# Optimization experiments

Hardware: AMD Instinct MI355X
Metric: run time of the kernel (lower is better)

The kernel has to match this reference:

```python
import jax, jax.numpy as jnp
import numpy as np

N = 750_000      # total nodes (10,000 graphs x 75 superpixels)
E = 6_000_000    # directed edges (avg degree 8)
G = 10_000       # number of graphs
NINP, H, HFC, NCLS = 2, 64, 32, 10
BN_EPS = 1e-5


def setup_inputs() -> dict:
    key = jax.random.key(0)
    ks = jax.random.split(key, 12)
    x = jax.random.normal(ks[0], (N, NINP), dtype=jnp.float32)
    edge_index = jax.random.randint(ks[1], (2, E), 0, N, dtype=jnp.int32)
    batch = jnp.sort(jax.random.randint(ks[2], (N,), 0, G, dtype=jnp.int32))
    def glorot(k, shape):
        fan_in, fan_out = shape
        s = jnp.sqrt(6.0 / (fan_in + fan_out)).astype(jnp.float32)
        return jax.random.uniform(k, shape, jnp.float32, -s, s)
    return {
        "x": x, "edge_index": edge_index, "batch": batch,
        "W1": glorot(ks[3], (NINP, H)), "b1": jnp.zeros((H,), jnp.float32),
        "W2": glorot(ks[4], (H, H)),    "b2": jnp.zeros((H,), jnp.float32),
        "W3": glorot(ks[5], (H, H)),    "b3": jnp.zeros((H,), jnp.float32),
        "gamma": jnp.ones((H,), jnp.float32), "beta": jnp.zeros((H,), jnp.float32),
        "fcW1": glorot(ks[6], (H, HFC)),  "fcb1": jnp.zeros((HFC,), jnp.float32),
        "fcW2": glorot(ks[7], (HFC, NCLS)), "fcb2": jnp.zeros((NCLS,), jnp.float32),
    }


def reference(x, edge_index, batch, W1, b1, W2, b2, W3, b3,
              gamma, beta, fcW1, fcb1, fcW2, fcb2):
    n = x.shape[0]
    loop = jnp.arange(n, dtype=edge_index.dtype)
    src = jnp.concatenate([edge_index[0], loop])   # [E+N] self-loops added
    dst = jnp.concatenate([edge_index[1], loop])
    # symmetric GCN normalization: deg from destination with unit edge weights
    deg = jax.ops.segment_sum(jnp.ones_like(dst, jnp.float32), dst, num_segments=n)
    dinv = jnp.where(deg > 0, jax.lax.rsqrt(deg), 0.0)
    norm = (dinv[src] * dinv[dst])[:, None]        # [E+N, 1]

    def gcn_conv(h, W, b):
        h = h @ W                                   # linear transform first (small K)
        msg = h[src] * norm                         # gather + normalize
        return jax.ops.segment_sum(msg, dst, num_segments=n) + b  # scatter-add

    h = jax.nn.relu(gcn_conv(x, W1, b1))
    h = jax.nn.relu(gcn_conv(h, W2, b2))
    h = jax.nn.relu(gcn_conv(h, W3, b3))

    # global mean pool over graphs
    sums = jax.ops.segment_sum(h, batch, num_segments=G)
    cnts = jax.ops.segment_sum(jnp.ones((n, 1), jnp.float32), batch, num_segments=G)
    pooled = sums / jnp.maximum(cnts, 1.0)          # [G, H]

    # BatchNorm1d (training mode: batch statistics, biased variance)
    mean = pooled.mean(axis=0)
    var = pooled.var(axis=0)
    hbn = (pooled - mean) * jax.lax.rsqrt(var + BN_EPS) * gamma + beta

    h = jax.nn.relu(hbn @ fcW1 + fcb1)
    logits = h @ fcW2 + fcb2
    return jax.nn.log_softmax(logits, axis=1)
```

## Files before the change

kernel.cpp:

```cpp
#include <hip/hip_runtime.h>
#include <hip/hip_fp16.h>

#define HDIM 64
#define HFC 32
#define NCLS 10
#define DT32 32
#define DT64 64

#define NBUCK 256
#define BSH   12
#define BUCKN 4096
#define EPT   16
#define CHUNK 4096
#define CAPSH 16
#define CAP   (1 << CAPSH)

__device__ inline __half2 u2h2(unsigned int u) {
    __half2 r;
    *reinterpret_cast<unsigned int*>(&r) = u;
    return r;
}
__device__ inline unsigned int h22u(__half2 h) {
    return *reinterpret_cast<unsigned int*>(&h);
}

__device__ inline __half2 h2relu(__half2 a) {
    unsigned int ua = h22u(a), uz = 0u, r;
    asm("v_pk_max_f16 %0, %1, %2" : "=v"(r) : "v"(ua), "v"(uz));
    return u2h2(r);
}

__device__ inline float fdot2u(unsigned int a, unsigned int b, float c) {
#if __has_builtin(__builtin_amdgcn_fdot2)
    typedef _Float16 f16x2 __attribute__((ext_vector_type(2)));
    union U { unsigned int u; f16x2 h; };
    U ua, ub; ua.u = a; ub.u = b;
    return __builtin_amdgcn_fdot2(ua.h, ub.h, c, false);
#else
    float2 fa = __half22float2(u2h2(a));
    float2 fb = __half22float2(u2h2(b));
    return fmaf(fa.x, fb.x, fmaf(fa.y, fb.y, c));
#endif
}


__global__ void k_initcur(int* __restrict__ gcur) {
    gcur[threadIdx.x] = threadIdx.x << CAPSH;
}

__global__ __launch_bounds__(256) void k_split(const int* __restrict__ src,
                                               const int* __restrict__ dst,
                                               int* __restrict__ gcur,
                                               unsigned int* __restrict__ part, int E) {
    __shared__ int cnt[NBUCK];
    __shared__ int off[NBUCK];
    cnt[threadIdx.x] = 0;
    __syncthreads();
    int base = blockIdx.x * CHUNK + threadIdx.x;
    int s16[EPT], d16[EPT], b16[EPT];
    #pragma unroll
    for (int i = 0; i < EPT; ++i) {
        int e = base + i * 256;
        bool ok = e < E;
        s16[i] = ok ? src[e] : 0;
        d16[i] = ok ? dst[e] : 0;
        b16[i] = ok ? (d16[i] >> BSH) : -1;
        if (ok) atomicAdd(&cnt[b16[i]], 1);
    }
    __syncthreads();
    {
        int c = cnt[threadIdx.x];
        off[threadIdx.x] = c ? atomicAdd(&gcur[threadIdx.x], c) : 0;
    }
    __syncthreads();
    #pragma unroll
    for (int i = 0; i < EPT; ++i) {
        if (b16[i] >= 0) {
            int slot = atomicAdd(&off[b16[i]], 1);
            part[slot] = ((unsigned)(d16[i] & (BUCKN - 1)) << 20) | (unsigned)s16[i];
        }
    }
}

__global__ __launch_bounds__(256) void k_build(const unsigned int* __restrict__ part,
                                               const int* __restrict__ gcur,
                                               unsigned int* __restrict__ begdeg,
                                               int* __restrict__ col, int n) {
    __shared__ int cnt[BUCKN];
    __shared__ int tmp[256];
    const int b = blockIdx.x;
    const int s = b << CAPSH, t = gcur[b];
    const int nodeBase = b << BSH;
    for (int i = threadIdx.x; i < BUCKN; i += 256) cnt[i] = 0;
    __syncthreads();
    for (int e = s + threadIdx.x; e < t; e += 256) {
        int local = (int)(part[e] >> 20);
        atomicAdd(&cnt[local], 1);
    }
    __syncthreads();
    int my[16]; int sum = 0;
    #pragma unroll
    for (int i = 0; i < 16; ++i) { my[i] = cnt[threadIdx.x * 16 + i]; sum += my[i]; }
    tmp[threadIdx.x] = sum; __syncthreads();
    for (int o = 1; o < 256; o <<= 1) {
        int v = ((int)threadIdx.x >= o) ? tmp[threadIdx.x - o] : 0;
        __syncthreads();
        tmp[threadIdx.x] += v;
        __syncthreads();
    }
    int run = tmp[threadIdx.x] - sum + s;
    __syncthreads();
    #pragma unroll
    for (int i = 0; i < 16; ++i) {
        int local = threadIdx.x * 16 + i;
        int node = nodeBase + local;
        int c = my[i];
        cnt[local] = run;
        if (node < n) begdeg[node] = ((unsigned)c << 24) | (unsigned)run;
        run += c;
    }
    __syncthreads();
    for (int e = s + threadIdx.x; e < t; e += 256) {
        unsigned int pe = part[e];
        int local = (int)(pe >> 20);
        int p = atomicAdd(&cnt[local], 1);
        col[p] = (int)(pe & 0xFFFFFu);
    }
}


__global__ void k_xs(const float* __restrict__ x, const unsigned int* __restrict__ begdeg,
                     unsigned int* __restrict__ xsh, int n) {
    int i = blockIdx.x * blockDim.x + threadIdx.x;
    if (i >= n) return;
    unsigned int bd = begdeg[i];
    float dv = rsqrtf((float)(bd >> 24) + 1.0f);
    float2 v = reinterpret_cast<const float2*>(x)[i];
    xsh[i] = h22u(__floats2half2_rn(v.x * dv, v.y * dv));
}

__global__ void k_gather1(const unsigned int* __restrict__ begdeg, const int* __restrict__ col,
                          const unsigned int* __restrict__ xsh,
                          uint2* __restrict__ aggd, int n) {
    int d = blockIdx.x * blockDim.x + threadIdx.x;
    if (d >= n) return;
    unsigned int bd = begdeg[d];
    int e0 = (int)(bd & 0xFFFFFFu);
    int deg = (int)(bd >> 24);
    int e1 = e0 + deg;
    float dv = rsqrtf((float)deg + 1.0f);
    float2 v = __half22float2(u2h2(xsh[d]));
    float a0 = v.x, a1 = v.y;
    int e = e0;
    for (; e + 4 <= e1; e += 4) {
        int c0 = col[e], c1 = col[e + 1], c2 = col[e + 2], c3 = col[e + 3];
        float2 w0 = __half22float2(u2h2(xsh[c0]));
        float2 w1 = __half22float2(u2h2(xsh[c1]));
        float2 w2 = __half22float2(u2h2(xsh[c2]));
        float2 w3 = __half22float2(u2h2(xsh[c3]));
        a0 += w0.x + w1.x + w2.x + w3.x;
        a1 += w0.y + w1.y + w2.y + w3.y;
    }
    for (; e < e1; ++e) {
        float2 w = __half22float2(u2h2(xsh[col[e]]));
        a0 += w.x; a1 += w.y;
    }
    uint2 o;
    o.x = h22u(__floats2half2_rn(a0 * dv, a1 * dv));
    o.y = h22u(__floats2half2_rn(dv, 0.0f));
    aggd[d] = o;
}

__global__ __launch_bounds__(256) void k_layer12(
        const unsigned int* __restrict__ begdeg, const int* __restrict__ col,
        const uint2* __restrict__ aggd,
        const float* __restrict__ W1, const float* __restrict__ b1,
        const float* __restrict__ W2, const float* __restrict__ b2,
        __half* __restrict__ out, int n) {
    __shared__ unsigned int sWp[HDIM / 2][HDIM];
    __shared__ float sB2[HDIM];
    __shared__ float sW1a[HDIM], sW1b[HDIM], sB1[HDIM];
    __shared__ unsigned int sAgg[DT64][HDIM / 2];
    __shared__ __half sOut[DT64][HDIM];

    for (int i = threadIdx.x; i < (HDIM / 2) * HDIM; i += 256) {
        int k2 = i >> 6, f = i & 63;
        sWp[k2][f] = h22u(__floats2half2_rn(W2[(2 * k2) * HDIM + f], W2[(2 * k2 + 1) * HDIM + f]));
    }
    if (threadIdx.x < HDIM) {
        sW1a[threadIdx.x] = W1[threadIdx.x];
        sW1b[threadIdx.x] = W1[HDIM + threadIdx.x];
        sB1[threadIdx.x] = b1[threadIdx.x];
        sB2[threadIdx.x] = b2[threadIdx.x];
    }
    __syncthreads();

    const int base = blockIdx.x * DT64;
    const int nValid = min(DT64, n - base);
    const int nd = threadIdx.x >> 2;
    const int q  = threadIdx.x & 3;
    const int node = base + nd;

    __half2 w1a2[8], w1b2[8], bb2[8];
    #pragma unroll
    for (int j = 0; j < 8; ++j) {
        int f = q * 16 + 2 * j;
        w1a2[j] = __floats2half2_rn(sW1a[f], sW1a[f + 1]);
        w1b2[j] = __floats2half2_rn(sW1b[f], sW1b[f + 1]);
        bb2[j]  = __floats2half2_rn(sB1[f], sB1[f + 1]);
    }

    if (nd < nValid) {
        __half2 acc[8];
        uint2 sv = aggd[node];
        __half2 zz = u2h2(sv.x);
        __half2 zx2 = __low2half2(zz), zy2 = __high2half2(zz);
        __half2 sd2 = __low2half2(u2h2(sv.y));
        #pragma unroll
        for (int j = 0; j < 8; ++j) {
            __half2 t = __hfma2(zx2, w1a2[j], __hfma2(zy2, w1b2[j], bb2[j]));
            acc[j] = __hmul2(h2relu(t), sd2);
        }
        unsigned int bd = begdeg[node];
        int e0 = (int)(bd & 0xFFFFFFu);
        int e1 = e0 + (int)(bd >> 24);
        int e = e0;
        for (; e + 4 <= e1; e += 4) {
            int c0 = col[e], c1 = col[e + 1], c2 = col[e + 2], c3 = col[e + 3];
            uint2 v0 = aggd[c0];
            uint2 v1 = aggd[c1];
            uint2 v2 = aggd[c2];
            uint2 v3 = aggd[c3];
            __half2 z0 = u2h2(v0.x), z1 = u2h2(v1.x), z2 = u2h2(v2.x), z3 = u2h2(v3.x);
            __half2 x0 = __low2half2(z0), y0 = __high2half2(z0), d0 = __low2half2(u2h2(v0.y));
            __half2 x1 = __low2half2(z1), y1 = __high2half2(z1), d1 = __low2half2(u2h2(v1.y));
            __half2 x2 = __low2half2(z2), y2 = __high2half2(z2), d2 = __low2half2(u2h2(v2.y));
            __half2 x3 = __low2half2(z3), y3 = __high2half2(z3), d3 = __low2half2(u2h2(v3.y));
            #pragma unroll
            for (int j = 0; j < 8; ++j) {
                __half2 t0 = __hfma2(x0, w1a2[j], __hfma2(y0, w1b2[j], bb2[j]));
                acc[j] = __hfma2(h2relu(t0), d0, acc[j]);
                __half2 t1 = __hfma2(x1, w1a2[j], __hfma2(y1, w1b2[j], bb2[j]));
                acc[j] = __hfma2(h2relu(t1), d1, acc[j]);
                __half2 t2 = __hfma2(x2, w1a2[j], __hfma2(y2, w1b2[j], bb2[j]));
                acc[j] = __hfma2(h2relu(t2), d2, acc[j]);
                __half2 t3 = __hfma2(x3, w1a2[j], __hfma2(y3, w1b2[j], bb2[j]));
                acc[j] = __hfma2(h2relu(t3), d3, acc[j]);
            }
        }
        for (; e < e1; ++e) {
            uint2 v0 = aggd[col[e]];
            __half2 z0 = u2h2(v0.x);
            __half2 x0 = __low2half2(z0), y0 = __high2half2(z0), d0 = __low2half2(u2h2(v0.y));
            #pragma unroll
            for (int j = 0; j < 8; ++j) {
                __half2 t0 = __hfma2(x0, w1a2[j], __hfma2(y0, w1b2[j], bb2[j]));
                acc[j] = __hfma2(h2relu(t0), d0, acc[j]);
            }
        }
        #pragma unroll
        for (int j = 0; j < 8; ++j) acc[j] = __hmul2(acc[j], sd2);
        uint4 o0, o1;
        o0.x = h22u(acc[0]); o0.y = h22u(acc[1]); o0.z = h22u(acc[2]); o0.w = h22u(acc[3]);
        o1.x = h22u(acc[4]); o1.y = h22u(acc[5]); o1.z = h22u(acc[6]); o1.w = h22u(acc[7]);
        uint4* sa = reinterpret_cast<uint4*>(&sAgg[nd][q * 8]);
        sa[0] = o0; sa[1] = o1;
    }
    __syncthreads();

    {
        const int f  = threadIdx.x & 63;
        const int ng = threadIdx.x >> 6;
        for (int ii = ng; ii < DT64; ii += 4) {
            int onode = base + ii;
            if (onode >= n) break;
            float acc = sB2[f];
            #pragma unroll
            for (int k2 = 0; k2 < HDIM / 2; ++k2)
                acc = fdot2u(sAgg[ii][k2], sWp[k2][f], acc);
            unsigned int bd = begdeg[onode];
            float sc = rsqrtf((float)(bd >> 24) + 1.0f);
            sOut[ii][f] = __float2half(fmaxf(acc, 0.0f) * sc);
        }
    }
    __syncthreads();

    if (nd < nValid) {
        const uint4* so = reinterpret_cast<const uint4*>(&sOut[nd][q * 16]);
        uint4* go = reinterpret_cast<uint4*>(out + (long long)node * HDIM + q * 16);
        go[0] = so[0];
        go[1] = so[1];
    }
}

__global__ __launch_bounds__(256) void k_layer64(
        const unsigned int* __restrict__ begdeg, const int* __restrict__ col,
        const __half* __restrict__ hs,
        const float* __restrict__ W, const float* __restrict__ b,
        const int* __restrict__ batchArr,
        float* __restrict__ pooled, int n) {
    __shared__ unsigned int sWp[HDIM / 2][HDIM];
    __shared__ float sB[HDIM];
    __shared__ unsigned int sAgg[DT32][HDIM / 2];
    __shared__ __half sOut[DT32][HDIM];
    __shared__ int sGid[DT32];

    for (int i = threadIdx.x; i < (HDIM / 2) * HDIM; i += 256) {
        int k2 = i >> 6, f = i & 63;
        sWp[k2][f] = h22u(__floats2half2_rn(W[(2 * k2) * HDIM + f], W[(2 * k2 + 1) * HDIM + f]));
    }
    if (threadIdx.x < HDIM) sB[threadIdx.x] = b[threadIdx.x];

    const int base = blockIdx.x * DT32;
    const int nValid = min(DT32, n - base);
    const int nd = threadIdx.x >> 3;
    const int q  = threadIdx.x & 7;
    const int node = base + nd;

    if (threadIdx.x < DT32)
        sGid[threadIdx.x] = (threadIdx.x < nValid) ? batchArr[base + threadIdx.x] : -1;

    if (nd < nValid) {
        const uint4* rows = reinterpret_cast<const uint4*>(hs);
        uint4 v = rows[(long long)node * 8 + q];
        __half2 a0 = u2h2(v.x), a1 = u2h2(v.y), a2 = u2h2(v.z), a3 = u2h2(v.w);
        __half2 b0 = u2h2(0u), b1 = u2h2(0u), b2 = u2h2(0u), b3 = u2h2(0u);
        unsigned int bd = begdeg[node];
        int e0 = (int)(bd & 0xFFFFFFu);
        int deg = (int)(bd >> 24);
        int e1 = e0 + deg;
        int e = e0;
        for (; e + 8 <= e1; e += 8) {
            int c0 = col[e], c1 = col[e + 1], c2 = col[e + 2], c3 = col[e + 3];
            int c4 = col[e + 4], c5 = col[e + 5], c6 = col[e + 6], c7 = col[e + 7];
            uint4 w0 = rows[(long long)c0 * 8 + q];
            uint4 w1 = rows[(long long)c1 * 8 + q];
            uint4 w2 = rows[(long long)c2 * 8 + q];
            uint4 w3 = rows[(long long)c3 * 8 + q];
            uint4 w4 = rows[(long long)c4 * 8 + q];
            uint4 w5 = rows[(long long)c5 * 8 + q];
            uint4 w6 = rows[(long long)c6 * 8 + q];
            uint4 w7 = rows[(long long)c7 * 8 + q];
            a0 = __hadd2(a0, u2h2(w0.x)); a1 = __hadd2(a1, u2h2(w0.y));
            a2 = __hadd2(a2, u2h2(w0.z)); a3 = __hadd2(a3, u2h2(w0.w));
            b0 = __hadd2(b0, u2h2(w1.x)); b1 = __hadd2(b1, u2h2(w1.y));
            b2 = __hadd2(b2, u2h2(w1.z)); b3 = __hadd2(b3, u2h2(w1.w));
            a0 = __hadd2(a0, u2h2(w2.x)); a1 = __hadd2(a1, u2h2(w2.y));
            a2 = __hadd2(a2, u2h2(w2.z)); a3 = __hadd2(a3, u2h2(w2.w));
            b0 = __hadd2(b0, u2h2(w3.x)); b1 = __hadd2(b1, u2h2(w3.y));
            b2 = __hadd2(b2, u2h2(w3.z)); b3 = __hadd2(b3, u2h2(w3.w));
            a0 = __hadd2(a0, u2h2(w4.x)); a1 = __hadd2(a1, u2h2(w4.y));
            a2 = __hadd2(a2, u2h2(w4.z)); a3 = __hadd2(a3, u2h2(w4.w));
            b0 = __hadd2(b0, u2h2(w5.x)); b1 = __hadd2(b1, u2h2(w5.y));
            b2 = __hadd2(b2, u2h2(w5.z)); b3 = __hadd2(b3, u2h2(w5.w));
            a0 = __hadd2(a0, u2h2(w6.x)); a1 = __hadd2(a1, u2h2(w6.y));
            a2 = __hadd2(a2, u2h2(w6.z)); a3 = __hadd2(a3, u2h2(w6.w));
            b0 = __hadd2(b0, u2h2(w7.x)); b1 = __hadd2(b1, u2h2(w7.y));
            b2 = __hadd2(b2, u2h2(w7.z)); b3 = __hadd2(b3, u2h2(w7.w));
        }
        for (; e + 4 <= e1; e += 4) {
            int c0 = col[e], c1 = col[e + 1], c2 = col[e + 2], c3 = col[e + 3];
            uint4 w0 = rows[(long long)c0 * 8 + q];
            uint4 w1 = rows[(long long)c1 * 8 + q];
            uint4 w2 = rows[(long long)c2 * 8 + q];
            uint4 w3 = rows[(long long)c3 * 8 + q];
            a0 = __hadd2(a0, u2h2(w0.x)); a1 = __hadd2(a1, u2h2(w0.y));
            a2 = __hadd2(a2, u2h2(w0.z)); a3 = __hadd2(a3, u2h2(w0.w));
            b0 = __hadd2(b0, u2h2(w1.x)); b1 = __hadd2(b1, u2h2(w1.y));
            b2 = __hadd2(b2, u2h2(w1.z)); b3 = __hadd2(b3, u2h2(w1.w));
            a0 = __hadd2(a0, u2h2(w2.x)); a1 = __hadd2(a1, u2h2(w2.y));
            a2 = __hadd2(a2, u2h2(w2.z)); a3 = __hadd2(a3, u2h2(w2.w));
            b0 = __hadd2(b0, u2h2(w3.x)); b1 = __hadd2(b1, u2h2(w3.y));
            b2 = __hadd2(b2, u2h2(w3.z)); b3 = __hadd2(b3, u2h2(w3.w));
        }
        for (; e < e1; ++e) {
            uint4 w = rows[(long long)col[e] * 8 + q];
            a0 = __hadd2(a0, u2h2(w.x)); a1 = __hadd2(a1, u2h2(w.y));
            a2 = __hadd2(a2, u2h2(w.z)); a3 = __hadd2(a3, u2h2(w.w));
        }
        a0 = __hadd2(a0, b0); a1 = __hadd2(a1, b1);
        a2 = __hadd2(a2, b2); a3 = __hadd2(a3, b3);
        float dv = rsqrtf((float)deg + 1.0f);
        float2 f0 = __half22float2(a0), f1 = __half22float2(a1);
        float2 f2 = __half22float2(a2), f3 = __half22float2(a3);
        uint4 o;
        o.x = h22u(__floats2half2_rn(f0.x * dv, f0.y * dv));
        o.y = h22u(__floats2half2_rn(f1.x * dv, f1.y * dv));
        o.z = h22u(__floats2half2_rn(f2.x * dv, f2.y * dv));
        o.w = h22u(__floats2half2_rn(f3.x * dv, f3.y * dv));
        *reinterpret_cast<uint4*>(&sAgg[nd][q * 4]) = o;
    }
    __syncthreads();

    {
        const int f  = threadIdx.x & 63;
        const int ng = threadIdx.x >> 6;
        for (int ii = ng; ii < DT32; ii += 4) {
            int onode = base + ii;
            if (onode >= n) break;
            float acc = sB[f];
            #pragma unroll
            for (int k2 = 0; k2 < HDIM / 2; ++k2)
                acc = fdot2u(sAgg[ii][k2], sWp[k2][f], acc);
            sOut[ii][f] = __float2half(fmaxf(acc, 0.0f));
        }
    }
    __syncthreads();

    if (threadIdx.x < HDIM) {
        int f = threadIdx.x;
        float acc = 0.0f;
        int prev = sGid[0];
        for (int ii = 0; ii < nValid; ++ii) {
            int g = sGid[ii];
            if (g != prev) {
                if (prev >= 0) atomicAdd(&pooled[(long long)prev * HDIM + f], acc);
                acc = 0.0f; prev = g;
            }
            acc += __half2float(sOut[ii][f]);
        }
        if (prev >= 0) atomicAdd(&pooled[(long long)prev * HDIM + f], acc);
    }
}


__global__ void k_start(const int* __restrict__ batch, int* __restrict__ startArr,
                        int n, int G) {
    int g = blockIdx.x * blockDim.x + threadIdx.x;
    if (g > G) return;
    int lo = 0, hi = n;
    while (lo < hi) {
        int mid = (lo + hi) >> 1;
        if (batch[mid] < g) lo = mid + 1; else hi = mid;
    }
    startArr[g] = lo;
}

__global__ void k_bnstats(const float* __restrict__ pooled, const int* __restrict__ startArr,
                          const float* __restrict__ gamma, const float* __restrict__ beta,
                          float* __restrict__ scale, float* __restrict__ shift, int G) {
    int f = blockIdx.x;
    __shared__ float ss[256], ss2[256];
    float s = 0.0f, s2 = 0.0f;
    for (int g = threadIdx.x; g < G; g += blockDim.x) {
        float c = (float)(startArr[g + 1] - startArr[g]);
        float v = pooled[(long long)g * HDIM + f] / fmaxf(c, 1.0f);
        s += v; s2 += v * v;
    }
    ss[threadIdx.x] = s; ss2[threadIdx.x] = s2;
    __syncthreads();
    for (int off = 128; off > 0; off >>= 1) {
        if (threadIdx.x < off) {
            ss[threadIdx.x]  += ss[threadIdx.x + off];
            ss2[threadIdx.x] += ss2[threadIdx.x + off];
        }
        __syncthreads();
    }
    if (threadIdx.x == 0) {
        float mean = ss[0] / (float)G;
        float var  = ss2[0] / (float)G - mean * mean;
        float rstd = rsqrtf(var + 1e-5f);
        float sc = gamma[f] * rstd;
        scale[f] = sc;
        shift[f] = beta[f] - mean * sc;
    }
}

__global__ void k_head(const float* __restrict__ pooled, const int* __restrict__ startArr,
                       const float* __restrict__ scale, const float* __restrict__ shift,
                       const float* __restrict__ fcW1, const float* __restrict__ fcb1,
                       const float* __restrict__ fcW2, const float* __restrict__ fcb2,
                       float* __restrict__ out, int G) {
    __shared__ float sW1[HDIM * HFC];
    __shared__ float sW2[HFC * NCLS];
    __shared__ float sb1[HFC], sb2[NCLS], ssc[HDIM], ssh[HDIM];
    for (int i = threadIdx.x; i < HDIM * HFC; i += blockDim.x) sW1[i] = fcW1[i];
    for (int i = threadIdx.x; i < HFC * NCLS; i += blockDim.x) sW2[i] = fcW2[i];
    if (threadIdx.x < HFC)  sb1[threadIdx.x] = fcb1[threadIdx.x];
    if (threadIdx.x < NCLS) sb2[threadIdx.x] = fcb2[threadIdx.x];
    if (threadIdx.x < HDIM) { ssc[threadIdx.x] = scale[threadIdx.x]; ssh[threadIdx.x] = shift[threadIdx.x]; }
    __syncthreads();
    int g = blockIdx.x * blockDim.x + threadIdx.x;
    if (g >= G) return;
    float inv = 1.0f / fmaxf((float)(startArr[g + 1] - startArr[g]), 1.0f);
    float bn[HDIM];
    #pragma unroll
    for (int f = 0; f < HDIM; ++f)
        bn[f] = pooled[(long long)g * HDIM + f] * inv * ssc[f] + ssh[f];
    float hfc[HFC];
    #pragma unroll
    for (int j = 0; j < HFC; ++j) {
        float a = sb1[j];
        #pragma unroll
        for (int f = 0; f < HDIM; ++f) a = fmaf(bn[f], sW1[f * HFC + j], a);
        hfc[j] = fmaxf(a, 0.0f);
    }
    float lg[NCLS];
    float mx = -1e30f;
    #pragma unroll
    for (int c = 0; c < NCLS; ++c) {
        float a = sb2[c];
        #pragma unroll
        for (int j = 0; j < HFC; ++j) a = fmaf(hfc[j], sW2[j * NCLS + c], a);
        lg[c] = a;
        mx = fmaxf(mx, a);
    }
    float se = 0.0f;
    #pragma unroll
    for (int c = 0; c < NCLS; ++c) se += expf(lg[c] - mx);
    float lse = mx + logf(se);
    #pragma unroll
    for (int c = 0; c < NCLS; ++c) out[(long long)g * NCLS + c] = lg[c] - lse;
}


static inline char* bump(char*& p, size_t bytes) {
    char* r = p;
    p += (bytes + 255) & ~(size_t)255;
    return r;
}

extern "C" void kernel_launch(void* const* d_in, const int* in_sizes, int n_in,
                              void* d_out, int out_size, void* d_ws, size_t ws_size,
                              hipStream_t stream) {
    const float* x     = (const float*)d_in[0];
    const int*   ei    = (const int*)d_in[1];
    const int*   batch = (const int*)d_in[2];
    const float* W1    = (const float*)d_in[3];
    const float* b1    = (const float*)d_in[4];
    const float* W2    = (const float*)d_in[5];
    const float* b2    = (const float*)d_in[6];
    const float* W3    = (const float*)d_in[7];
    const float* b3    = (const float*)d_in[8];
    const float* gamma = (const float*)d_in[9];
    const float* beta  = (const float*)d_in[10];
    const float* fcW1  = (const float*)d_in[11];
    const float* fcb1  = (const float*)d_in[12];
    const float* fcW2  = (const float*)d_in[13];
    const float* fcb2  = (const float*)d_in[14];

    const long long n = in_sizes[2];
    const int ni = (int)n;
    const int E = in_sizes[1] / 2;
    const int G = out_size / NCLS;
    const int* src = ei;
    const int* dst = ei + E;
    const int B = 256;

    char* p = (char*)d_ws;
    int*          gcur   = (int*)bump(p, NBUCK * 4);
    unsigned int* begdeg = (unsigned int*)bump(p, n * 4);
    int*          startA = (int*)bump(p, (size_t)(G + 1) * 4);
    float*        pooled = (float*)bump(p, (size_t)G * HDIM * 4);
    float*        scale  = (float*)bump(p, 2 * HDIM * 4);
    float*        shift  = scale + HDIM;
    unsigned int* xsh    = (unsigned int*)bump(p, n * 4);
    uint2*        aggd   = (uint2*)bump(p, (size_t)n * 8);
    char*         R      = bump(p, (size_t)HDIM * n * 2);
    int*          col    = (int*)bump(p, (size_t)NBUCK * CAP * 4);

    unsigned int* part = (unsigned int*)R;
    __half* hB = (__half*)R;

    (void)hipMemsetAsync(pooled, 0, (size_t)G * HDIM * 4, stream);

    const int nchunk = (E + CHUNK - 1) / CHUNK;
    const int nbU = (ni + BUCKN - 1) >> BSH;
    k_initcur<<<1, NBUCK, 0, stream>>>(gcur);
    k_split<<<nchunk, B, 0, stream>>>(src, dst, gcur, part, E);
    k_build<<<nbU, B, 0, stream>>>(part, gcur, begdeg, col, ni);

    k_start<<<(G + 1 + B - 1) / B, B, 0, stream>>>(batch, startA, ni, G);

    k_xs<<<(ni + B - 1) / B, B, 0, stream>>>(x, begdeg, xsh, ni);
    k_gather1<<<(ni + B - 1) / B, B, 0, stream>>>(begdeg, col, xsh, aggd, ni);

    const int nblk64 = (ni + DT64 - 1) / DT64;
    k_layer12<<<nblk64, B, 0, stream>>>(begdeg, col, aggd, W1, b1, W2, b2, hB, ni);

    const int nblk32 = (ni + DT32 - 1) / DT32;
    k_layer64<<<nblk32, B, 0, stream>>>(begdeg, col, hB, W3, b3, batch, pooled, ni);

    k_bnstats<<<HDIM, B, 0, stream>>>(pooled, startA, gamma, beta, scale, shift, G);
    k_head<<<(G + B - 1) / B, B, 0, stream>>>(pooled, startA, scale, shift,
                                              fcW1, fcb1, fcW2, fcb2, (float*)d_out, G);
}
```

Before: 581.1 us.

## Fuse xs scaling into CSR build, widen gather unroll, pad shared arrays

Folds the per-node degree-scaled half conversion of x into k_build, removing the separate k_xs launch and its re-read of begdeg. The gather loops in k_gather1 and k_layer12 are unrolled to 8 edges with two independent accumulators, so more loads are in flight and the add dependency chains are shorter. The shared sAgg/sOut arrays in the layer kernels get row padding to reduce LDS bank conflicts. The wider unroll raises register pressure, and in k_build the x reads are strided across threads, so they coalesce poorly.

```diff
diff --git a/kernel.cpp b/kernel.cpp
--- a/kernel.cpp
+++ b/kernel.cpp
@@ -84,7 +84,9 @@
 
 __global__ __launch_bounds__(256) void k_build(const unsigned int* __restrict__ part,
                                                const int* __restrict__ gcur,
+                                               const float* __restrict__ x,
                                                unsigned int* __restrict__ begdeg,
+                                               unsigned int* __restrict__ xsh,
                                                int* __restrict__ col, int n) {
     __shared__ int cnt[BUCKN];
     __shared__ int tmp[256];
@@ -116,7 +118,12 @@
         int node = nodeBase + local;
         int c = my[i];
         cnt[local] = run;
-        if (node < n) begdeg[node] = ((unsigned)c << 24) | (unsigned)run;
+        if (node < n) {
+            begdeg[node] = ((unsigned)c << 24) | (unsigned)run;
+            float dv = rsqrtf((float)c + 1.0f);
+            float2 v = reinterpret_cast<const float2*>(x)[node];
+            xsh[node] = h22u(__floats2half2_rn(v.x * dv, v.y * dv));
+        }
         run += c;
     }
     __syncthreads();
@@ -128,16 +135,6 @@
     }
 }
 
-
-__global__ void k_xs(const float* __restrict__ x, const unsigned int* __restrict__ begdeg,
-                     unsigned int* __restrict__ xsh, int n) {
-    int i = blockIdx.x * blockDim.x + threadIdx.x;
-    if (i >= n) return;
-    unsigned int bd = begdeg[i];
-    float dv = rsqrtf((float)(bd >> 24) + 1.0f);
-    float2 v = reinterpret_cast<const float2*>(x)[i];
-    xsh[i] = h22u(__floats2half2_rn(v.x * dv, v.y * dv));
-}
 
 __global__ void k_gather1(const unsigned int* __restrict__ begdeg, const int* __restrict__ col,
                           const unsigned int* __restrict__ xsh,
@@ -151,20 +148,29 @@
     float dv = rsqrtf((float)deg + 1.0f);
     float2 v = __half22float2(u2h2(xsh[d]));
     float a0 = v.x, a1 = v.y;
+    float b0 = 0.0f, b1 = 0.0f;
     int e = e0;
-    for (; e + 4 <= e1; e += 4) {
+    for (; e + 8 <= e1; e += 8) {
         int c0 = col[e], c1 = col[e + 1], c2 = col[e + 2], c3 = col[e + 3];
+        int c4 = col[e + 4], c5 = col[e + 5], c6 = col[e + 6], c7 = col[e + 7];
         float2 w0 = __half22float2(u2h2(xsh[c0]));
         float2 w1 = __half22float2(u2h2(xsh[c1]));
         float2 w2 = __half22float2(u2h2(xsh[c2]));
         float2 w3 = __half22float2(u2h2(xsh[c3]));
-        a0 += w0.x + w1.x + w2.x + w3.x;
-        a1 += w0.y + w1.y + w2.y + w3.y;
+        float2 w4 = __half22float2(u2h2(xsh[c4]));
+        float2 w5 = __half22float2(u2h2(xsh[c5]));
+        float2 w6 = __half22float2(u2h2(xsh[c6]));
+        float2 w7 = __half22float2(u2h2(xsh[c7]));
+        a0 += w0.x + w2.x + w4.x + w6.x;
+        a1 += w0.y + w2.y + w4.y + w6.y;
+        b0 += w1.x + w3.x + w5.x + w7.x;
+        b1 += w1.y + w3.y + w5.y + w7.y;
     }
     for (; e < e1; ++e) {
         float2 w = __half22float2(u2h2(xsh[col[e]]));
         a0 += w.x; a1 += w.y;
     }
+    a0 += b0; a1 += b1;
     uint2 o;
     o.x = h22u(__floats2half2_rn(a0 * dv, a1 * dv));
     o.y = h22u(__floats2half2_rn(dv, 0.0f));
@@ -180,8 +186,8 @@
     __shared__ unsigned int sWp[HDIM / 2][HDIM];
     __shared__ float sB2[HDIM];
     __shared__ float sW1a[HDIM], sW1b[HDIM], sB1[HDIM];
-    __shared__ unsigned int sAgg[DT64][HDIM / 2];
-    __shared__ __half sOut[DT64][HDIM];
+    __shared__ unsigned int sAgg[DT64][HDIM / 2 + 4];
+    __shared__ __half sOut[DT64][HDIM + 8];
 
     for (int i = threadIdx.x; i < (HDIM / 2) * HDIM; i += 256) {
         int k2 = i >> 6, f = i & 63;
@@ -211,7 +217,7 @@
     }
 
     if (nd < nValid) {
-        __half2 acc[8];
+        __half2 accA[8], accB[8];
         uint2 sv = aggd[node];
         __half2 zz = u2h2(sv.x);
         __half2 zx2 = __low2half2(zz), zy2 = __high2half2(zz);
@@ -219,12 +225,54 @@
         #pragma unroll
         for (int j = 0; j < 8; ++j) {
             __half2 t = __hfma2(zx2, w1a2[j], __hfma2(zy2, w1b2[j], bb2[j]));
-            acc[j] = __hmul2(h2relu(t), sd2);
+            accA[j] = __hmul2(h2relu(t), sd2);
+            accB[j] = u2h2(0u);
         }
         unsigned int bd = begdeg[node];
         int e0 = (int)(bd & 0xFFFFFFu);
         int e1 = e0 + (int)(bd >> 24);
         int e = e0;
+        for (; e + 8 <= e1; e += 8) {
+            int c0 = col[e], c1 = col[e + 1], c2 = col[e + 2], c3 = col[e + 3];
+            int c4 = col[e + 4], c5 = col[e + 5], c6 = col[e + 6], c7 = col[e + 7];
+            uint2 v0 = aggd[c0];
+            uint2 v1 = aggd[c1];
+            uint2 v2 = aggd[c2];
+            uint2 v3 = aggd[c3];
+            uint2 v4 = aggd[c4];
+            uint2 v5 = aggd[c5];
+            uint2 v6 = aggd[c6];
+            uint2 v7 = aggd[c7];
+            __half2 z0 = u2h2(v0.x), z1 = u2h2(v1.x), z2 = u2h2(v2.x), z3 = u2h2(v3.x);
+            __half2 z4 = u2h2(v4.x), z5 = u2h2(v5.x), z6 = u2h2(v6.x), z7 = u2h2(v7.x);
+            __half2 x0 = __low2half2(z0), y0 = __high2half2(z0), d0 = __low2half2(u2h2(v0.y));
+            __half2 x1 = __low2half2(z1), y1 = __high2half2(z1), d1 = __low2half2(u2h2(v1.y));
+            __half2 x2 = __low2half2(z2), y2 = __high2half2(z2), d2 = __low2half2(u2h2(v2.y));
+            __half2 x3 = __low2half2(z3), y3 = __high2half2(z3), d3 = __low2half2(u2h2(v3.y));
+            __half2 x4 = __low2half2(z4), y4 = __high2half2(z4), d4 = __low2half2(u2h2(v4.y));
+            __half2 x5 = __low2half2(z5), y5 = __high2half2(z5), d5 = __low2half2(u2h2(v5.y));
+            __half2 x6 = __low2half2(z6), y6 = __high2half2(z6), d6 = __low2half2(u2h2(v6.y));
+            __half2 x7 = __low2half2(z7), y7 = __high2half2(z7), d7 = __low2half2(u2h2(v7.y));
+            #pragma unroll
+            for (int j = 0; j < 8; ++j) {
+                __half2 t0 = __hfma2(x0, w1a2[j], __hfma2(y0, w1b2[j], bb2[j]));
+                accA[j] = __hfma2(h2relu(t0), d0, accA[j]);
+                __half2 t1 = __hfma2(x1, w1a2[j], __hfma2(y1, w1b2[j], bb2[j]));
+                accB[j] = __hfma2(h2relu(t1), d1, accB[j]);
+                __half2 t2 = __hfma2(x2, w1a2[j], __hfma2(y2, w1b2[j], bb2[j]));
+                accA[j] = __hfma2(h2relu(t2), d2, accA[j]);
+                __half2 t3 = __hfma2(x3, w1a2[j], __hfma2(y3, w1b2[j], bb2[j]));
+                accB[j] = __hfma2(h2relu(t3), d3, accB[j]);
+                __half2 t4 = __hfma2(x4, w1a2[j], __hfma2(y4, w1b2[j], bb2[j]));
+                accA[j] = __hfma2(h2relu(t4), d4, accA[j]);
+                __half2 t5 = __hfma2(x5, w1a2[j], __hfma2(y5, w1b2[j], bb2[j]));
+                accB[j] = __hfma2(h2relu(t5), d5, accB[j]);
+                __half2 t6 = __hfma2(x6, w1a2[j], __hfma2(y6, w1b2[j], bb2[j]));
+                accA[j] = __hfma2(h2relu(t6), d6, accA[j]);
+                __half2 t7 = __hfma2(x7, w1a2[j], __hfma2(y7, w1b2[j], bb2[j]));
+                accB[j] = __hfma2(h2relu(t7), d7, accB[j]);
+            }
+        }
         for (; e + 4 <= e1; e += 4) {
             int c0 = col[e], c1 = col[e + 1], c2 = col[e + 2], c3 = col[e + 3];
             uint2 v0 = aggd[c0];
@@ -239,13 +287,13 @@
             #pragma unroll
             for (int j = 0; j < 8; ++j) {
                 __half2 t0 = __hfma2(x0, w1a2[j], __hfma2(y0, w1b2[j], bb2[j]));
-                acc[j] = __hfma2(h2relu(t0), d0, acc[j]);
+                accA[j] = __hfma2(h2relu(t0), d0, accA[j]);
                 __half2 t1 = __hfma2(x1, w1a2[j], __hfma2(y1, w1b2[j], bb2[j]));
-                acc[j] = __hfma2(h2relu(t1), d1, acc[j]);
+                accB[j] = __hfma2(h2relu(t1), d1, accB[j]);
                 __half2 t2 = __hfma2(x2, w1a2[j], __hfma2(y2, w1b2[j], bb2[j]));
-                acc[j] = __hfma2(h2relu(t2), d2, acc[j]);
+                accA[j] = __hfma2(h2relu(t2), d2, accA[j]);
                 __half2 t3 = __hfma2(x3, w1a2[j], __hfma2(y3, w1b2[j], bb2[j]));
-                acc[j] = __hfma2(h2relu(t3), d3, acc[j]);
+                accB[j] = __hfma2(h2relu(t3), d3, accB[j]);
             }
         }
         for (; e < e1; ++e) {
@@ -255,14 +303,15 @@
             #pragma unroll
             for (int j = 0; j < 8; ++j) {
                 __half2 t0 = __hfma2(x0, w1a2[j], __hfma2(y0, w1b2[j], bb2[j]));
-                acc[j] = __hfma2(h2relu(t0), d0, acc[j]);
+                accA[j] = __hfma2(h2relu(t0), d0, accA[j]);
             }
         }
         #pragma unroll
-        for (int j = 0; j < 8; ++j) acc[j] = __hmul2(acc[j], sd2);
+        for (int j = 0; j < 8; ++j)
+            accA[j] = __hmul2(__hadd2(accA[j], accB[j]), sd2);
         uint4 o0, o1;
-        o0.x = h22u(acc[0]); o0.y = h22u(acc[1]); o0.z = h22u(acc[2]); o0.w = h22u(acc[3]);
-        o1.x = h22u(acc[4]); o1.y = h22u(acc[5]); o1.z = h22u(acc[6]); o1.w = h22u(acc[7]);
+        o0.x = h22u(accA[0]); o0.y = h22u(accA[1]); o0.z = h22u(accA[2]); o0.w = h22u(accA[3]);
+        o1.x = h22u(accA[4]); o1.y = h22u(accA[5]); o1.z = h22u(accA[6]); o1.w = h22u(accA[7]);
         uint4* sa = reinterpret_cast<uint4*>(&sAgg[nd][q * 8]);
         sa[0] = o0; sa[1] = o1;
     }
@@ -301,8 +350,8 @@
         float* __restrict__ pooled, int n) {
     __shared__ unsigned int sWp[HDIM / 2][HDIM];
     __shared__ float sB[HDIM];
-    __shared__ unsigned int sAgg[DT32][HDIM / 2];
-    __shared__ __half sOut[DT32][HDIM];
+    __shared__ unsigned int sAgg[DT32][HDIM / 2 + 4];
+    __shared__ __half sOut[DT32][HDIM + 8];
     __shared__ int sGid[DT32];
 
     for (int i = threadIdx.x; i < (HDIM / 2) * HDIM; i += 256) {
@@ -568,11 +617,10 @@
     const int nbU = (ni + BUCKN - 1) >> BSH;
     k_initcur<<<1, NBUCK, 0, stream>>>(gcur);
     k_split<<<nchunk, B, 0, stream>>>(src, dst, gcur, part, E);
-    k_build<<<nbU, B, 0, stream>>>(part, gcur, begdeg, col, ni);
+    k_build<<<nbU, B, 0, stream>>>(part, gcur, x, begdeg, xsh, col, ni);
 
     k_start<<<(G + 1 + B - 1) / B, B, 0, stream>>>(batch, startA, ni, G);
 
-    k_xs<<<(ni + B - 1) / B, B, 0, stream>>>(x, begdeg, xsh, ni);
     k_gather1<<<(ni + B - 1) / B, B, 0, stream>>>(begdeg, col, xsh, aggd, ni);
 
     const int nblk64 = (ni + DT64 - 1) / DT64;
```

Result: no change. 574.3 us (-1.2%).
